# Kernel tuning notes

Hardware: AMD Instinct MI355X
Metric: run time of the kernel (lower is better)

## Reference

```python
import jax, jax.numpy as jnp
import numpy as np

N = 49998      # num nodes, divisible by (neg_sample_ratio + 2) = 3
E = 800000     # num edges (avg degree 16)
DIM_IN = 128
DIM_OUT = 32
H0 = 8         # heads layer 0
H1 = 1         # heads layer 1


def setup_inputs() -> dict:
    key = jax.random.key(0)
    ks = jax.random.split(key, 16)
    s = 0.05
    x = jax.random.normal(ks[0], (N, DIM_IN), dtype=jnp.float32)
    src = jax.random.randint(ks[1], (E,), 0, N)
    dst = jax.random.randint(ks[2], (E,), 0, N)
    W0 = jax.random.normal(ks[3], (DIM_IN, H0 * DIM_OUT), dtype=jnp.float32) * s
    al0 = jax.random.normal(ks[4], (H0, DIM_OUT), dtype=jnp.float32) * s
    ar0 = jax.random.normal(ks[5], (H0, DIM_OUT), dtype=jnp.float32) * s
    b0 = jnp.zeros((H0 * DIM_OUT,), dtype=jnp.float32)
    W1 = jax.random.normal(ks[6], (H0 * DIM_OUT, H1 * DIM_OUT), dtype=jnp.float32) * s
    al1 = jax.random.normal(ks[7], (H1, DIM_OUT), dtype=jnp.float32) * s
    ar1 = jax.random.normal(ks[8], (H1, DIM_OUT), dtype=jnp.float32) * s
    b1 = jnp.zeros((H1 * DIM_OUT,), dtype=jnp.float32)
    P1 = jax.random.normal(ks[9], (DIM_OUT, DIM_OUT), dtype=jnp.float32) * s
    pb1 = jnp.zeros((DIM_OUT,), dtype=jnp.float32)
    P2 = jax.random.normal(ks[10], (DIM_OUT, DIM_OUT), dtype=jnp.float32) * s
    pb2 = jnp.zeros((DIM_OUT,), dtype=jnp.float32)
    P3 = jax.random.normal(ks[11], (DIM_OUT, 1), dtype=jnp.float32) * s
    pb3 = jnp.zeros((1,), dtype=jnp.float32)
    return dict(x=x, src=src, dst=dst, neg_sample_ratio=1,
                W0=W0, al0=al0, ar0=ar0, b0=b0,
                W1=W1, al1=al1, ar1=ar1, b1=b1,
                P1=P1, pb1=pb1, P2=P2, pb2=pb2, P3=P3, pb3=pb3)


def gat_conv(x, src, dst, W, al, ar, b):
    """DGL GATConv: linear proj -> edge LeakyReLU score -> per-dst segment softmax -> weighted scatter-sum + bias."""
    n = x.shape[0]
    H, D = al.shape
    f = (x @ W).reshape(n, H, D)                     # [N,H,D]
    el = jnp.sum(f * al, axis=-1)                    # [N,H]
    er = jnp.sum(f * ar, axis=-1)                    # [N,H]
    e = jax.nn.leaky_relu(el[src] + er[dst], 0.2)    # [E,H] edge scores
    m = jax.ops.segment_max(e, dst, num_segments=n)  # [N,H] stable softmax max
    a = jnp.exp(e - m[dst])                          # [E,H]
    denom = jax.ops.segment_sum(a, dst, num_segments=n)  # [N,H]
    a = a / denom[dst]                               # normalized attention
    out = jax.ops.segment_sum(a[:, :, None] * f[src], dst, num_segments=n)  # [N,H,D]
    return out + b.reshape(1, H, D)


def reference(x, src, dst, neg_sample_ratio,
              W0, al0, ar0, b0, W1, al1, ar1, b1,
              P1, pb1, P2, pb2, P3, pb3):
    # layer 0: GATConv with ELU activation, flatten heads
    h = jax.nn.elu(gat_conv(x, src, dst, W0, al0, ar0, b0)).reshape(x.shape[0], -1)
    # layer 1: GATConv, no activation, mean over heads
    h = gat_conv(h, src, dst, W1, al1, ar1, b1).mean(axis=1)  # [N, DIM_OUT]

    num_edge = h.shape[0] // (neg_sample_ratio + 2)
    src_h = h[:num_edge]
    pos_dst_h = h[num_edge:2 * num_edge]
    neg_dst_h = h[2 * num_edge:]

    def predictor(z):
        z = jax.nn.relu(z @ P1 + pb1)
        z = jax.nn.relu(z @ P2 + pb2)
        return z @ P3 + pb3

    h_pos = predictor(src_h * pos_dst_h)
    h_neg = predictor(jnp.tile(src_h, (neg_sample_ratio, 1)) * neg_dst_h)
    return (h_pos, h_neg)
```

## Files before the change

kernel.cpp:

```cpp
#include <hip/hip_runtime.h>
#include <hip/hip_fp16.h>
#include <cmath>

#define CAPB 64
#define CAPF 88
#define CAP1 96
#define WA   92
#define G0_ROWS 64
#define G0_PAD 68

typedef _Float16 h2v __attribute__((ext_vector_type(2)));

__device__ __forceinline__ float dot2a(unsigned f, unsigned w, float acc) {
  return __builtin_amdgcn_fdot2(__builtin_bit_cast(h2v, f),
                                __builtin_bit_cast(h2v, w), acc, false);
}
__device__ __forceinline__ unsigned pkh2(float lo, float hi) {
  return (unsigned)__half_as_ushort(__float2half_rn(lo)) |
         ((unsigned)__half_as_ushort(__float2half_rn(hi)) << 16);
}

__global__ void k_prep(const float* __restrict__ W0, const float* __restrict__ W1,
                       unsigned* __restrict__ W0h, unsigned* __restrict__ W1ct,
                       int* __restrict__ cnt, int Np1) {
  int gid = blockIdx.x * 256 + threadIdx.x;
  int stride = gridDim.x * 256;
  for (int i = gid; i < Np1; i += stride) cnt[i] = 0;
  if (gid < 16384) {
    int k2 = gid >> 8, c = gid & 255;
    W0h[gid] = pkh2(W0[(size_t)(2 * k2) * 256 + c], W0[(size_t)(2 * k2 + 1) * 256 + c]);
  } else if (gid < 20480) {
    int j = gid - 16384;
    int c = j >> 7, k2 = j & 127;
    W1ct[j] = pkh2(W1[(size_t)(2 * k2) * 32 + c], W1[(size_t)(2 * k2 + 1) * 32 + c]);
  } else if (gid < 20992) {
    W0h[gid - 20992 + 16896] = 0;
  }
}

__global__ void k_gemm0_scatter(const float* __restrict__ x, const unsigned* __restrict__ W0h,
                                const float* __restrict__ al, const float* __restrict__ ar,
                                const int* __restrict__ dst, const int* __restrict__ src,
                                unsigned short* __restrict__ f0h, float* __restrict__ el,
                                float* __restrict__ er, int* __restrict__ cnt,
                                int* __restrict__ ovf_cnt, int* __restrict__ bpad,
                                int* __restrict__ ovf, int N, int E, int ngemm) {
  __shared__ unsigned s_x2[66 * G0_PAD];
  int t = threadIdx.x;

  if (blockIdx.x >= ngemm) {
    int nscat = gridDim.x - ngemm;
    for (int e = (blockIdx.x - ngemm) * blockDim.x + t; e < E; e += nscat * blockDim.x) {
      int d = dst[e];
      int pos = atomicAdd(&cnt[d], 1);
      if (pos < CAPB) bpad[(size_t)d * CAPB + pos] = src[e];
      else { int op = atomicAdd(ovf_cnt, 1); ovf[op] = e; }
    }
    return;
  }

  int w = t >> 6, l = t & 63;
  int row0 = blockIdx.x * G0_ROWS;
  {
    int row = row0 + l; if (row >= N) row = N - 1;
    const float* xp = x + (size_t)row * 128 + w * 32;
#pragma unroll
    for (int j = 0; j < 8; ++j) {
      float4 v = *(const float4*)(xp + 4 * j);
      int k2 = w * 16 + 2 * j;
      s_x2[k2 * G0_PAD + l] = pkh2(v.x, v.y);
      s_x2[(k2 + 1) * G0_PAD + l] = pkh2(v.z, v.w);
    }
  }
  __syncthreads();

  float4 acc[16];
#pragma unroll
  for (int r = 0; r < 16; ++r) acc[r] = make_float4(0.f, 0.f, 0.f, 0.f);

  const unsigned* wp = W0h + 4 * l;
  int rbase = w * 16;

#define LDX(dstv, kk)                                              \
  { const unsigned* xk_ = &s_x2[(kk) * G0_PAD + rbase];            \
    *(uint4*)&dstv[0]  = *(const uint4*)(xk_);                     \
    *(uint4*)&dstv[4]  = *(const uint4*)(xk_ + 4);                 \
    *(uint4*)&dstv[8]  = *(const uint4*)(xk_ + 8);                 \
    *(uint4*)&dstv[12] = *(const uint4*)(xk_ + 12); }
#define DOTS(xv, w4)                                               \
  _Pragma("unroll")                                                \
  for (int r = 0; r < 16; ++r) {                                   \
    acc[r].x = dot2a(xv[r], w4.x, acc[r].x);                       \
    acc[r].y = dot2a(xv[r], w4.y, acc[r].y);                       \
    acc[r].z = dot2a(xv[r], w4.z, acc[r].z);                       \
    acc[r].w = dot2a(xv[r], w4.w, acc[r].w);                       \
  }

  unsigned xA[16], xB[16];
  uint4 wA = *(const uint4*)(wp);
  LDX(xA, 0);
  for (int k2 = 0; k2 < 64; k2 += 2) {
    uint4 wB = *(const uint4*)(wp + (size_t)(k2 + 1) * 256);
    LDX(xB, k2 + 1);
    DOTS(xA, wA);
    wA = *(const uint4*)(wp + (size_t)(k2 + 2) * 256);
    LDX(xA, k2 + 2);
    DOTS(xB, wB);
  }
#undef LDX
#undef DOTS

  int hh = l >> 3;
  float4 al4 = *(const float4*)(al + 4 * l);
  float4 ar4 = *(const float4*)(ar + 4 * l);
#pragma unroll
  for (int r = 0; r < 16; ++r) {
    int row = row0 + rbase + r;
    float4 f = acc[r];
    if (row < N) {
      ushort4 h4;
      h4.x = __half_as_ushort(__float2half_rn(f.x));
      h4.y = __half_as_ushort(__float2half_rn(f.y));
      h4.z = __half_as_ushort(__float2half_rn(f.z));
      h4.w = __half_as_ushort(__float2half_rn(f.w));
      *(ushort4*)(f0h + (size_t)row * 256 + 4 * l) = h4;
    }
    float pl = fmaf(f.x, al4.x, fmaf(f.y, al4.y, fmaf(f.z, al4.z, f.w * al4.w)));
    float pr = fmaf(f.x, ar4.x, fmaf(f.y, ar4.y, fmaf(f.z, ar4.z, f.w * ar4.w)));
#pragma unroll
    for (int off = 4; off >= 1; off >>= 1) {
      pl += __shfl_xor(pl, off, 64);
      pr += __shfl_xor(pr, off, 64);
    }
    if ((l & 7) == 0 && row < N) {
      el[row * 8 + hh] = pl;
      er[row * 8 + hh] = pr;
    }
  }
}

__global__ void k_fused0(const float* __restrict__ el, const float* __restrict__ er,
                         const unsigned short* __restrict__ f0h, const int* __restrict__ cnt,
                         const int* __restrict__ ovf_cnt, const int* __restrict__ bpad,
                         const int* __restrict__ ovf, const int* __restrict__ dstp,
                         const int* __restrict__ src, const float* __restrict__ b0,
                         const unsigned* __restrict__ W1ct, const float* __restrict__ al1,
                         const float* __restrict__ ar1, unsigned short* __restrict__ f1h,
                         float* __restrict__ el1, float* __restrict__ er1, int N) {
  __shared__ unsigned s_w1[32 * 132];
  __shared__ unsigned short s_wa[8][8 * WA];
  __shared__ int s_s[8][CAPF];
  __shared__ unsigned s_h2[8][128];

  const int t = threadIdx.x;
  for (int base = t * 4; base < 4096; base += 2048) {
    uint4 v = *(const uint4*)&W1ct[base];
    int c = base >> 7, k2 = base & 127;
    *(uint4*)&s_w1[c * 132 + k2] = v;
  }
  __syncthreads();

  const int w = __builtin_amdgcn_readfirstlane(t >> 6);
  const int l = t & 63;
  const int n = blockIdx.x * 8 + w;
  if (n >= N) return;

  int* sS = s_s[w];
  unsigned short* sWA = s_wa[w];

  const int sub = l & 31, half = l >> 5, hh = sub >> 2;
  float4 b0a = ((const float4*)(b0 + 8 * sub))[0];
  float4 b0b = ((const float4*)(b0 + 8 * sub))[1];
  float al1c = al1[sub], ar1c = ar1[sub];

  int cn = cnt[n];
  int degb = cn < CAPB ? cn : CAPB;
  if (l < degb) sS[l] = bpad[(size_t)n * CAPB + l];
  int deg = degb;
  int ovl = ovf_cnt[0];
  if (ovl) {
    int d = degb;
    if (l == 0) {
      for (int j = 0; j < ovl && d < 84; ++j) {
        int e = ovf[j];
        if (dstp[e] == n) sS[d++] = src[e];
      }
    }
    deg = __shfl(d, 0, 64);
  }

  int degp = (deg + 3) & ~3;
  if (l < degp - deg) sS[deg + l] = sS[0];

  uint4 A, B;
  int2 sp;
  if (degp > 0) {
    sp = *(const int2*)&sS[2 * half];
    A = ((const uint4*)(f0h + (size_t)sp.x * 256))[sub];
    B = ((const uint4*)(f0h + (size_t)sp.y * 256))[sub];
  }

  float er_h = er[n * 8 + (l & 7)];
  float psum = 0.f;
  for (int e = l >> 3; e < deg; e += 8) {
    int sidx = sS[e];
    float v = el[sidx * 8 + (l & 7)] + er_h;
    v = v >= 0.f ? v : 0.2f * v;
    float a = __expf(v);
    sWA[(l & 7) * WA + e] = __half_as_ushort(__float2half_rn(a));
    psum += a;
  }
  psum += __shfl_xor(psum, 8, 64);
  psum += __shfl_xor(psum, 16, 64);
  psum += __shfl_xor(psum, 32, 64);
  float rs = psum > 0.f ? __builtin_amdgcn_rcpf(psum) : 0.f;

  { int pe = deg + (l >> 3); if (pe < degp) sWA[(l & 7) * WA + pe] = 0; }

  float a0 = 0.f, a1 = 0.f, a2 = 0.f, a3 = 0.f, a4 = 0.f, a5 = 0.f, a6 = 0.f, a7 = 0.f;
  if (degp > 0) {
    for (int i = 0;;) {
      int in = i + 4;
      uint4 A2, B2;
      if (in < degp) {
        int2 s2 = *(const int2*)&sS[in + 2 * half];
        A2 = ((const uint4*)(f0h + (size_t)s2.x * 256))[sub];
        B2 = ((const uint4*)(f0h + (size_t)s2.y * 256))[sub];
      }
      unsigned wp = *(const unsigned*)&sWA[hh * WA + i + 2 * half];
      unsigned lo, hi;
      lo = __builtin_amdgcn_perm(A.x, B.x, 0x01000504u);
      hi = __builtin_amdgcn_perm(A.x, B.x, 0x03020706u);
      a0 = dot2a(lo, wp, a0); a1 = dot2a(hi, wp, a1);
      lo = __builtin_amdgcn_perm(A.y, B.y, 0x01000504u);
      hi = __builtin_amdgcn_perm(A.y, B.y, 0x03020706u);
      a2 = dot2a(lo, wp, a2); a3 = dot2a(hi, wp, a3);
      lo = __builtin_amdgcn_perm(A.z, B.z, 0x01000504u);
      hi = __builtin_amdgcn_perm(A.z, B.z, 0x03020706u);
      a4 = dot2a(lo, wp, a4); a5 = dot2a(hi, wp, a5);
      lo = __builtin_amdgcn_perm(A.w, B.w, 0x01000504u);
      hi = __builtin_amdgcn_perm(A.w, B.w, 0x03020706u);
      a6 = dot2a(lo, wp, a6); a7 = dot2a(hi, wp, a7);
      if (in >= degp) break;
      i = in; A = A2; B = B2;
    }
  }
  a0 += __shfl_xor(a0, 32, 64); a1 += __shfl_xor(a1, 32, 64);
  a2 += __shfl_xor(a2, 32, 64); a3 += __shfl_xor(a3, 32, 64);
  a4 += __shfl_xor(a4, 32, 64); a5 += __shfl_xor(a5, 32, 64);
  a6 += __shfl_xor(a6, 32, 64); a7 += __shfl_xor(a7, 32, 64);

  float sc = __shfl(rs, hh, 64);
  float o0 = fmaf(a0, sc, b0a.x), o1 = fmaf(a1, sc, b0a.y);
  float o2 = fmaf(a2, sc, b0a.z), o3 = fmaf(a3, sc, b0a.w);
  float o4 = fmaf(a4, sc, b0b.x), o5 = fmaf(a5, sc, b0b.y);
  float o6 = fmaf(a6, sc, b0b.z), o7 = fmaf(a7, sc, b0b.w);
  o0 = o0 > 0.f ? o0 : __expf(o0) - 1.f;  o1 = o1 > 0.f ? o1 : __expf(o1) - 1.f;
  o2 = o2 > 0.f ? o2 : __expf(o2) - 1.f;  o3 = o3 > 0.f ? o3 : __expf(o3) - 1.f;
  o4 = o4 > 0.f ? o4 : __expf(o4) - 1.f;  o5 = o5 > 0.f ? o5 : __expf(o5) - 1.f;
  o6 = o6 > 0.f ? o6 : __expf(o6) - 1.f;  o7 = o7 > 0.f ? o7 : __expf(o7) - 1.f;
  if (half == 0) {
    uint4 hp;
    hp.x = pkh2(o0, o1); hp.y = pkh2(o2, o3);
    hp.z = pkh2(o4, o5); hp.w = pkh2(o6, o7);
    *(uint4*)&s_h2[w][4 * sub] = hp;
  }
  asm volatile("s_waitcnt lgkmcnt(0)" ::: "memory");

  const unsigned* wrow = &s_w1[sub * 132 + half * 64];
  const unsigned* hrow = &s_h2[w][half * 64];
  float p = 0.f;
#pragma unroll
  for (int j = 0; j < 64; j += 4) {
    uint4 wv = *(const uint4*)&wrow[j];
    uint4 hv = *(const uint4*)&hrow[j];
    p = dot2a(hv.x, wv.x, p);
    p = dot2a(hv.y, wv.y, p);
    p = dot2a(hv.z, wv.z, p);
    p = dot2a(hv.w, wv.w, p);
  }
  p += __shfl_xor(p, 32, 64);
  float pn = __shfl_xor(p, 1, 64);
  float pl = p * al1c, pr = p * ar1c;
#pragma unroll
  for (int off = 16; off >= 1; off >>= 1) {
    pl += __shfl_xor(pl, off, 64);
    pr += __shfl_xor(pr, off, 64);
  }
  if (half == 0 && (sub & 1) == 0)
    *(unsigned*)(f1h + (size_t)n * 32 + sub) = pkh2(p, pn);
  if (l == 0) { el1[n] = pl; er1[n] = pr; }
}

__global__ void k_fused1(const float* __restrict__ el, const float* __restrict__ er,
                         const unsigned short* __restrict__ f1h, const int* __restrict__ cnt,
                         const int* __restrict__ ovf_cnt, const int* __restrict__ bpad,
                         const int* __restrict__ ovf, const int* __restrict__ dstp,
                         const int* __restrict__ src, const float* __restrict__ b1,
                         float* __restrict__ h1, int N) {
  __shared__ int s_s[4][CAP1];
  __shared__ unsigned s_wp[4][CAP1 / 2];

  const int t = threadIdx.x;
  const int g = __builtin_amdgcn_readfirstlane(t >> 6);
  const int lane = t & 63;
  int n = blockIdx.x * 4 + g;
  int nn = n < N ? n : N - 1;
  int* sS = s_s[g];
  unsigned* sWP = s_wp[g];

  int cn = cnt[nn];
  int degb = cn < CAPB ? cn : CAPB;
  if (lane < degb) sS[lane] = bpad[(size_t)nn * CAPB + lane];
  int deg = degb;
  int ovl = ovf_cnt[0];
  if (ovl) {
    int d = degb;
    if (lane == 0) {
      for (int j = 0; j < ovl && d < CAP1 - 16; ++j) {
        int e = ovf[j];
        if (dstp[e] == nn) sS[d++] = src[e];
      }
    }
    deg = __shfl(d, 0, 64);
  }
  int degp = (deg + 15) & ~15;
  if (deg + lane < degp) sS[deg + lane] = sS[0];

  const int es = lane >> 3, q = lane & 7;
  uint2 A, B;
  if (degp > 0) {
    A = *(const uint2*)(f1h + (size_t)sS[es] * 32 + 4 * q);
    B = *(const uint2*)(f1h + (size_t)sS[es + 8] * 32 + 4 * q);
  }

  float er_n = er[nn];
  float psum = 0.f;
  for (int i0 = 0; i0 < degp; i0 += 64) {
    int i = i0 + lane;
    float a = 0.f;
    if (i < deg) {
      float v = el[sS[i]] + er_n;
      v = v >= 0.f ? v : 0.2f * v;
      a = __expf(v);
      psum += a;
    }
    float an = __shfl_xor(a, 8, 64);
    if ((lane & 15) < 8 && i < degp)
      sWP[(i0 >> 1) + ((lane >> 4) << 3) + (lane & 7)] = pkh2(a, an);
  }
#pragma unroll
  for (int off = 32; off >= 1; off >>= 1) psum += __shfl_xor(psum, off, 64);
  float rs = psum > 0.f ? __builtin_amdgcn_rcpf(psum) : 0.f;

  float c0 = 0.f, c1 = 0.f, c2 = 0.f, c3 = 0.f;
  if (degp > 0) {
    for (int i0 = 0;;) {
      int in = i0 + 16;
      uint2 A2, B2;
      if (in < degp) {
        A2 = *(const uint2*)(f1h + (size_t)sS[in + es] * 32 + 4 * q);
        B2 = *(const uint2*)(f1h + (size_t)sS[in + es + 8] * 32 + 4 * q);
      }
      unsigned wp = sWP[(i0 >> 1) + es];
      unsigned lo = __builtin_amdgcn_perm(A.x, B.x, 0x01000504u);
      unsigned hi = __builtin_amdgcn_perm(A.x, B.x, 0x03020706u);
      c0 = dot2a(lo, wp, c0); c1 = dot2a(hi, wp, c1);
      lo = __builtin_amdgcn_perm(A.y, B.y, 0x01000504u);
      hi = __builtin_amdgcn_perm(A.y, B.y, 0x03020706u);
      c2 = dot2a(lo, wp, c2); c3 = dot2a(hi, wp, c3);
      if (in >= degp) break;
      i0 = in; A = A2; B = B2;
    }
  }
#pragma unroll
  for (int off = 8; off <= 32; off <<= 1) {
    c0 += __shfl_xor(c0, off, 64); c1 += __shfl_xor(c1, off, 64);
    c2 += __shfl_xor(c2, off, 64); c3 += __shfl_xor(c3, off, 64);
  }
  if (es == 0 && n < N) {
    float4 b = *(const float4*)(b1 + 4 * q);
    float4 o;
    o.x = fmaf(c0, rs, b.x); o.y = fmaf(c1, rs, b.y);
    o.z = fmaf(c2, rs, b.z); o.w = fmaf(c3, rs, b.w);
    ((float4*)(h1 + (size_t)n * 32))[q] = o;
  }
}

__global__ void k_pred(const float* __restrict__ h1, const float* __restrict__ P1,
                       const float* __restrict__ pb1, const float* __restrict__ P2,
                       const float* __restrict__ pb2, const float* __restrict__ P3,
                       const float* __restrict__ pb3, float* __restrict__ out,
                       int num_edge, int total) {
  int t = threadIdx.x;
  int lane = t & 31, grp = t >> 5;
  int k = blockIdx.x * 8 + grp;
  int kk = k < total ? k : 0;
  float z;
  if (kk < num_edge) {
    z = h1[(size_t)kk * 32 + lane] * h1[(size_t)(kk + num_edge) * 32 + lane];
  } else {
    int i = kk - num_edge;
    z = h1[(size_t)(i % num_edge) * 32 + lane] * h1[(size_t)(2 * num_edge + i) * 32 + lane];
  }
  double a1 = 0;
#pragma unroll
  for (int d = 0; d < 32; ++d)
    a1 += (double)__shfl(z, d, 32) * (double)P1[d * 32 + lane];
  float t1 = (float)(a1 + (double)pb1[lane]);
  t1 = t1 > 0.f ? t1 : 0.f;
  double a2 = 0;
#pragma unroll
  for (int d = 0; d < 32; ++d)
    a2 += (double)__shfl(t1, d, 32) * (double)P2[d * 32 + lane];
  float t2 = (float)(a2 + (double)pb2[lane]);
  t2 = t2 > 0.f ? t2 : 0.f;
  double a3 = (double)t2 * (double)P3[lane];
#pragma unroll
  for (int off = 16; off >= 1; off >>= 1) a3 += __shfl_xor(a3, off, 64);
  if (lane == 0 && k < total) out[k] = (float)(a3 + (double)pb3[0]);
}

extern "C" void kernel_launch(void* const* d_in, const int* in_sizes, int n_in,
                              void* d_out, int out_size, void* d_ws, size_t ws_size,
                              hipStream_t stream) {
  const float* x   = (const float*)d_in[0];
  const int*   src = (const int*)d_in[1];
  const int*   dst = (const int*)d_in[2];
  const float* W0  = (const float*)d_in[4];
  const float* al0 = (const float*)d_in[5];
  const float* ar0 = (const float*)d_in[6];
  const float* b0  = (const float*)d_in[7];
  const float* W1  = (const float*)d_in[8];
  const float* al1 = (const float*)d_in[9];
  const float* ar1 = (const float*)d_in[10];
  const float* b1  = (const float*)d_in[11];
  const float* P1  = (const float*)d_in[12];
  const float* pb1 = (const float*)d_in[13];
  const float* P2  = (const float*)d_in[14];
  const float* pb2 = (const float*)d_in[15];
  const float* P3  = (const float*)d_in[16];
  const float* pb3 = (const float*)d_in[17];

  int N = in_sizes[0] / 128;
  int E = in_sizes[1];
  int num_edge = N - out_size;

  size_t off = 0;
  auto alloc = [&](size_t bytes) -> void* {
    void* p = (char*)d_ws + off;
    off += (bytes + 255) & ~(size_t)255;
    return p;
  };
  unsigned short* f0h = (unsigned short*)alloc((size_t)N * 256 * 2);
  unsigned short* f1h = (unsigned short*)alloc((size_t)N * 32 * 2);
  float* h1   = (float*)alloc((size_t)N * 32 * 4);
  float* el   = (float*)alloc((size_t)N * 8 * 4);
  float* er   = (float*)alloc((size_t)N * 8 * 4);
  float* el1  = (float*)alloc((size_t)N * 4);
  float* er1  = (float*)alloc((size_t)N * 4);
  int*   cnt  = (int*)alloc((size_t)(N + 1) * 4);
  int*   bpad = (int*)alloc((size_t)N * CAPB * 4);
  int*   ovf  = (int*)alloc((size_t)E * 4);
  unsigned* W1ct = (unsigned*)alloc(4096 * 4);
  unsigned* W0h  = (unsigned*)alloc(16896 * 4);
  if (off > ws_size) return;
  int* ovf_cnt = cnt + N;

  int ngemm = (N + G0_ROWS - 1) / G0_ROWS;
  k_prep<<<128, 256, 0, stream>>>(W0, W1, W0h, W1ct, cnt, N + 1);
  k_gemm0_scatter<<<1792, 256, 0, stream>>>(x, W0h, al0, ar0, dst, src,
                                            f0h, el, er, cnt, ovf_cnt, bpad, ovf,
                                            N, E, ngemm);
  k_fused0<<<(N + 7) / 8, 512, 0, stream>>>(el, er, f0h, cnt, ovf_cnt, bpad, ovf, dst,
                                            src, b0, W1ct, al1, ar1, f1h, el1, er1, N);
  k_fused1<<<(N + 3) / 4, 256, 0, stream>>>(el1, er1, f1h, cnt, ovf_cnt, bpad, ovf, dst,
                                            src, b1, h1, N);
  k_pred<<<(out_size + 7) / 8, 256, 0, stream>>>(h1, P1, pb1, P2, pb2, P3, pb3,
                                                 (float*)d_out, num_edge, out_size);
}
```

Before: 269.4 us.

## Deepen load prefetch in GEMM and gather loops, enlarge fused1 blocks

The layer-0 GEMM loop now prefetches weight vectors two k-steps ahead and is unrolled by two. The fused0 neighbor-gather loop is double-buffered, keeping two gathers in flight, to hide global load latency. k_fused1 runs 8 nodes per 512-thread block instead of 4 per 256. k_pred replaces a modulo with subtraction. Deeper prefetch raises register pressure, which could lower occupancy.

```diff
diff --git a/kernel.cpp b/kernel.cpp
--- a/kernel.cpp
+++ b/kernel.cpp
@@ -98,14 +98,17 @@
 
   unsigned xA[16], xB[16];
   uint4 wA = *(const uint4*)(wp);
+  uint4 wB = *(const uint4*)(wp + 256);
   LDX(xA, 0);
+#pragma unroll 2
   for (int k2 = 0; k2 < 64; k2 += 2) {
-    uint4 wB = *(const uint4*)(wp + (size_t)(k2 + 1) * 256);
+    uint4 wC = *(const uint4*)(wp + (size_t)(k2 + 2) * 256);
+    uint4 wD = *(const uint4*)(wp + (size_t)(k2 + 3) * 256);
     LDX(xB, k2 + 1);
     DOTS(xA, wA);
-    wA = *(const uint4*)(wp + (size_t)(k2 + 2) * 256);
     LDX(xA, k2 + 2);
     DOTS(xB, wB);
+    wA = wC; wB = wD;
   }
 #undef LDX
 #undef DOTS
@@ -192,12 +195,30 @@
   int degp = (deg + 3) & ~3;
   if (l < degp - deg) sS[deg + l] = sS[0];
 
-  uint4 A, B;
-  int2 sp;
+#define GLOAD(AA, BB, ii)                                              \
+  { int2 s_ = *(const int2*)&sS[(ii) + 2 * half];                      \
+    AA = ((const uint4*)(f0h + (size_t)s_.x * 256))[sub];              \
+    BB = ((const uint4*)(f0h + (size_t)s_.y * 256))[sub]; }
+#define GCOMP(AA, BB, ii)                                              \
+  { unsigned wpk = *(const unsigned*)&sWA[hh * WA + (ii) + 2 * half];  \
+    unsigned lo_, hi_;                                                 \
+    lo_ = __builtin_amdgcn_perm(AA.x, BB.x, 0x01000504u);              \
+    hi_ = __builtin_amdgcn_perm(AA.x, BB.x, 0x03020706u);              \
+    a0 = dot2a(lo_, wpk, a0); a1 = dot2a(hi_, wpk, a1);                \
+    lo_ = __builtin_amdgcn_perm(AA.y, BB.y, 0x01000504u);              \
+    hi_ = __builtin_amdgcn_perm(AA.y, BB.y, 0x03020706u);              \
+    a2 = dot2a(lo_, wpk, a2); a3 = dot2a(hi_, wpk, a3);                \
+    lo_ = __builtin_amdgcn_perm(AA.z, BB.z, 0x01000504u);              \
+    hi_ = __builtin_amdgcn_perm(AA.z, BB.z, 0x03020706u);              \
+    a4 = dot2a(lo_, wpk, a4); a5 = dot2a(hi_, wpk, a5);                \
+    lo_ = __builtin_amdgcn_perm(AA.w, BB.w, 0x01000504u);              \
+    hi_ = __builtin_amdgcn_perm(AA.w, BB.w, 0x03020706u);              \
+    a6 = dot2a(lo_, wpk, a6); a7 = dot2a(hi_, wpk, a7); }
+
+  uint4 A, B, A2, B2;
   if (degp > 0) {
-    sp = *(const int2*)&sS[2 * half];
-    A = ((const uint4*)(f0h + (size_t)sp.x * 256))[sub];
-    B = ((const uint4*)(f0h + (size_t)sp.y * 256))[sub];
+    GLOAD(A, B, 0);
+    if (degp > 4) GLOAD(A2, B2, 4);
   }
 
   float er_h = er[n * 8 + (l & 7)];
@@ -220,31 +241,17 @@
   float a0 = 0.f, a1 = 0.f, a2 = 0.f, a3 = 0.f, a4 = 0.f, a5 = 0.f, a6 = 0.f, a7 = 0.f;
   if (degp > 0) {
     for (int i = 0;;) {
-      int in = i + 4;
-      uint4 A2, B2;
-      if (in < degp) {
-        int2 s2 = *(const int2*)&sS[in + 2 * half];
-        A2 = ((const uint4*)(f0h + (size_t)s2.x * 256))[sub];
-        B2 = ((const uint4*)(f0h + (size_t)s2.y * 256))[sub];
-      }
-      unsigned wp = *(const unsigned*)&sWA[hh * WA + i + 2 * half];
-      unsigned lo, hi;
-      lo = __builtin_amdgcn_perm(A.x, B.x, 0x01000504u);
-      hi = __builtin_amdgcn_perm(A.x, B.x, 0x03020706u);
-      a0 = dot2a(lo, wp, a0); a1 = dot2a(hi, wp, a1);
-      lo = __builtin_amdgcn_perm(A.y, B.y, 0x01000504u);
-      hi = __builtin_amdgcn_perm(A.y, B.y, 0x03020706u);
-      a2 = dot2a(lo, wp, a2); a3 = dot2a(hi, wp, a3);
-      lo = __builtin_amdgcn_perm(A.z, B.z, 0x01000504u);
-      hi = __builtin_amdgcn_perm(A.z, B.z, 0x03020706u);
-      a4 = dot2a(lo, wp, a4); a5 = dot2a(hi, wp, a5);
-      lo = __builtin_amdgcn_perm(A.w, B.w, 0x01000504u);
-      hi = __builtin_amdgcn_perm(A.w, B.w, 0x03020706u);
-      a6 = dot2a(lo, wp, a6); a7 = dot2a(hi, wp, a7);
-      if (in >= degp) break;
-      i = in; A = A2; B = B2;
-    }
-  }
+      GCOMP(A, B, i);
+      if (i + 8 < degp) GLOAD(A, B, i + 8);
+      if (i + 4 >= degp) break;
+      GCOMP(A2, B2, i + 4);
+      if (i + 12 < degp) GLOAD(A2, B2, i + 12);
+      if (i + 8 >= degp) break;
+      i += 8;
+    }
+  }
+#undef GLOAD
+#undef GCOMP
   a0 += __shfl_xor(a0, 32, 64); a1 += __shfl_xor(a1, 32, 64);
   a2 += __shfl_xor(a2, 32, 64); a3 += __shfl_xor(a3, 32, 64);
   a4 += __shfl_xor(a4, 32, 64); a5 += __shfl_xor(a5, 32, 64);
@@ -298,13 +305,13 @@
                          const int* __restrict__ ovf, const int* __restrict__ dstp,
                          const int* __restrict__ src, const float* __restrict__ b1,
                          float* __restrict__ h1, int N) {
-  __shared__ int s_s[4][CAP1];
-  __shared__ unsigned s_wp[4][CAP1 / 2];
+  __shared__ int s_s[8][CAP1];
+  __shared__ unsigned s_wp[8][CAP1 / 2];
 
   const int t = threadIdx.x;
   const int g = __builtin_amdgcn_readfirstlane(t >> 6);
   const int lane = t & 63;
-  int n = blockIdx.x * 4 + g;
+  int n = blockIdx.x * 8 + g;
   int nn = n < N ? n : N - 1;
   int* sS = s_s[g];
   unsigned* sWP = s_wp[g];
@@ -401,7 +408,9 @@
     z = h1[(size_t)kk * 32 + lane] * h1[(size_t)(kk + num_edge) * 32 + lane];
   } else {
     int i = kk - num_edge;
-    z = h1[(size_t)(i % num_edge) * 32 + lane] * h1[(size_t)(2 * num_edge + i) * 32 + lane];
+    int im = i;
+    while (im >= num_edge) im -= num_edge;
+    z = h1[(size_t)im * 32 + lane] * h1[(size_t)(2 * num_edge + i) * 32 + lane];
   }
   double a1 = 0;
 #pragma unroll
@@ -474,7 +483,7 @@
                                             N, E, ngemm);
   k_fused0<<<(N + 7) / 8, 512, 0, stream>>>(el, er, f0h, cnt, ovf_cnt, bpad, ovf, dst,
                                             src, b0, W1ct, al1, ar1, f1h, el1, er1, N);
-  k_fused1<<<(N + 3) / 4, 256, 0, stream>>>(el1, er1, f1h, cnt, ovf_cnt, bpad, ovf, dst,
+  k_fused1<<<(N + 7) / 8, 512, 0, stream>>>(el1, er1, f1h, cnt, ovf_cnt, bpad, ovf, dst,
                                             src, b1, h1, N);
   k_pred<<<(out_size + 7) / 8, 256, 0, stream>>>(h1, P1, pb1, P2, pb2, P3, pb3,
                                                  (float*)d_out, num_edge, out_size);
```

Result: no change. 266.8 us (-1.0%).
